# Kernel tuning notes

Hardware: AMD Instinct MI355X
Metric: run time of the kernel (lower is better)

## Reference

```python
import jax, jax.numpy as jnp
import numpy as np

L = 10      # LSTM layers
H = 128     # hidden size
ENC = 4096  # traffic_encoder_output_len
B = 8192    # batch
T = 12      # points_to_predict
NUM_MODES = 25


def setup_inputs() -> dict:
    key = jax.random.key(0)
    ks = jax.random.split(key, 10)
    s = 1.0 / np.sqrt(H)
    return {
        "backbone_encoded": jax.random.normal(ks[0], (B, ENC), jnp.float32),
        "fc_in_W": jax.random.normal(ks[1], (H, ENC), jnp.float32) / np.sqrt(ENC),
        "fc_in_b": jax.random.normal(ks[2], (H,), jnp.float32) * s,
        "Wih": jax.random.normal(ks[3], (L, 4 * H, H), jnp.float32) * s,
        "Whh": jax.random.normal(ks[4], (L, 4 * H, H), jnp.float32) * s,
        "bih": jax.random.normal(ks[5], (L, 4 * H), jnp.float32) * s,
        "bhh": jax.random.normal(ks[6], (L, 4 * H), jnp.float32) * s,
        "fc_out_W": jax.random.normal(ks[7], (3 * NUM_MODES, H), jnp.float32) * s,
        "fc_out_b": jax.random.normal(ks[8], (3 * NUM_MODES,), jnp.float32) * s,
        "points_to_predict": T,
    }


def _lstm_stack(x, Wih, Whh, bih, bhh):
    # x: [B, T, H]; PyTorch gate order: i, f, g, o
    def run_layer(x, l):
        def step(carry, xt):
            h, c = carry
            gates = xt @ Wih[l].T + h @ Whh[l].T + bih[l] + bhh[l]  # [B, 4H]
            i, f, g, o = jnp.split(gates, 4, axis=-1)
            c = jax.nn.sigmoid(f) * c + jax.nn.sigmoid(i) * jnp.tanh(g)
            h = jax.nn.sigmoid(o) * jnp.tanh(c)
            return (h, c), h
        b = x.shape[0]
        h0 = jnp.zeros((b, H), x.dtype)
        _, ys = jax.lax.scan(step, (h0, h0), jnp.swapaxes(x, 0, 1))  # [T, B, H]
        return jnp.swapaxes(ys, 0, 1)

    for l in range(L):
        x = run_layer(x, l)
    return x


def reference(backbone_encoded, fc_in_W, fc_in_b, Wih, Whh, bih, bhh,
              fc_out_W, fc_out_b, points_to_predict):
    enc = jax.nn.relu(backbone_encoded @ fc_in_W.T + fc_in_b)        # [B, H]
    x = jnp.repeat(enc[:, None, :], points_to_predict, axis=1)      # [B, T, H]
    y = _lstm_stack(x, Wih, Whh, bih, bhh)                           # [B, T, H]
    fc = y @ fc_out_W.T + fc_out_b                                   # [B, T, 75]
    b, t, _ = fc.shape
    # chunk(25, dim=channels) of consecutive pairs -> [B, 25, T, 2]
    predictions = fc[:, :, :50].reshape(b, t, NUM_MODES, 2).transpose(0, 2, 1, 3)
    probabilities = jax.nn.softmax(fc[:, -1, 50:], axis=-1)          # [B, 25]
    return predictions, probabilities
```

## Files before the change

kernel.cpp:

```cpp
#include <hip/hip_runtime.h>

typedef _Float16 h16;
typedef _Float16 h4 __attribute__((ext_vector_type(4)));
typedef _Float16 h8 __attribute__((ext_vector_type(8)));
typedef float f4 __attribute__((ext_vector_type(4)));

#define NB 8192
#define NENC 4096
#define NH 128
#define NL 10
#define NT 12
#define PAD 136

#define OFF_FCIN 0
#define SZ_FCIN (128*4096)
#define OFF_W (OFF_FCIN + SZ_FCIN)
#define SZ_W (10*2*512*128)
#define OFF_FCOUT (OFF_W + SZ_W)
#define SZ_FCOUT (80*128)
#define OFF_ENC (OFF_FCOUT + SZ_FCOUT)
#define SZ_ENC (8192*128)
#define OFF_GX0 (OFF_ENC + SZ_ENC)
#define SZ_GX0 (8192*512)
#define BYTE_BIAS ((OFF_GX0 + SZ_GX0)*2)

__device__ __forceinline__ f4 splat4(float v) { f4 r; r[0]=v; r[1]=v; r[2]=v; r[3]=v; return r; }
__device__ __forceinline__ h8 cvt8(float4 a, float4 b) {
  h8 r; r[0]=(h16)a.x; r[1]=(h16)a.y; r[2]=(h16)a.z; r[3]=(h16)a.w;
  r[4]=(h16)b.x; r[5]=(h16)b.y; r[6]=(h16)b.z; r[7]=(h16)b.w; return r;
}

__device__ __forceinline__ h16 cell(float iv, float fv, float gv, float ov, float& c) {
  float ei = __builtin_amdgcn_exp2f(-1.4426950408889634f * iv);
  float ef = __builtin_amdgcn_exp2f(-1.4426950408889634f * fv);
  float eg = __builtin_amdgcn_exp2f(-2.8853900817779268f * gv);
  float eo = __builtin_amdgcn_exp2f(-1.4426950408889634f * ov);
  float ai = 1.f + ei, af = 1.f + ef, ag = 1.f + eg;
  float m1 = ai * ag;
  float R1 = __builtin_amdgcn_rcpf(af * m1);
  float cc = R1 * fmaf(af, 1.f - eg, c * m1);
  c = cc;
  float ec = __builtin_amdgcn_exp2f(-2.8853900817779268f * cc);
  float R2 = __builtin_amdgcn_rcpf((1.f + eo) * (1.f + ec));
  return (h16)(R2 * (1.f - ec));
}

__global__ __launch_bounds__(256) void prep(const float* __restrict__ fcinW,
                                            const float* __restrict__ Wih,
                                            const float* __restrict__ Whh,
                                            const float* __restrict__ bih,
                                            const float* __restrict__ bhh,
                                            const float* __restrict__ fcoutW,
                                            h16* __restrict__ wsh,
                                            float* __restrict__ wbias) {
  int idx = blockIdx.x * 256 + threadIdx.x;
  if (idx < 65536) {
    int r = idx >> 9, k8 = idx & 511;
    const float* src = fcinW + r * 4096 + k8 * 8;
    h8 v = cvt8(*(const float4*)src, *(const float4*)(src + 4));
    *(h8*)(wsh + OFF_FCIN + (((r >> 4) * 512 + k8) * 128 + (r & 15) * 8)) = v;
  } else if (idx < 229376) {
    int rel = idx - 65536;
    int l = rel >> 14, rr = rel & 16383;
    int ssel = rr >> 13, rk8 = rr & 8191;
    int r = rk8 >> 4, k8 = rk8 & 15;
    const float* src = (ssel ? Whh : Wih) + l * 65536 + r * 128 + k8 * 8;
    h8 v = cvt8(*(const float4*)src, *(const float4*)(src + 4));
    *(h8*)(wsh + OFF_W + (l * 2 + ssel) * 65536 +
           (((r >> 4) * 16 + k8) * 128 + (r & 15) * 8)) = v;
  } else if (idx < 230656) {
    int rel = idx - 229376;
    int r = rel >> 4, k8 = rel & 15;
    h8 v;
    if (r < 75) {
      const float* src = fcoutW + r * 128 + k8 * 8;
      v = cvt8(*(const float4*)src, *(const float4*)(src + 4));
    } else {
      for (int j = 0; j < 8; ++j) v[j] = (h16)0.f;
    }
    *(h8*)(wsh + OFF_FCOUT + (((r >> 4) * 16 + k8) * 128 + (r & 15) * 8)) = v;
  } else if (idx < 235776) {
    int rel = idx - 230656;
    wbias[rel] = bih[rel] + bhh[rel];
  }
}

__global__ __launch_bounds__(256) void kin(const float* __restrict__ A,
                                           const float* __restrict__ bvec,
                                           h16* __restrict__ wsh) {
  const h16* Wp = wsh + OFF_FCIN;
  h16* ench = wsh + OFF_ENC;
  int tid = threadIdx.x;
  int w = tid >> 6, lane = tid & 63, s = lane & 15, q = lane >> 4;
  int m0 = blockIdx.x * 16;
  int c0 = w * 32 + s, c1 = c0 + 16;
  f4 acc0 = splat4(bvec[c0]);
  f4 acc1 = splat4(bvec[c1]);
  const float* arow = A + (size_t)(m0 + s) * NENC;
  const h16* wp0 = Wp + (w * 2 + 0) * (512 * 128) + s * 8;
  const h16* wp1 = Wp + (w * 2 + 1) * (512 * 128) + s * 8;
#pragma unroll 4
  for (int kb = 0; kb < 128; ++kb) {
    int k0 = kb * 32 + q * 8;
    float4 x0 = *(const float4*)(arow + k0);
    float4 x1 = *(const float4*)(arow + k0 + 4);
    h8 af = cvt8(x0, x1);
    h8 b0 = *(const h8*)(wp0 + (kb * 4 + q) * 128);
    h8 b1 = *(const h8*)(wp1 + (kb * 4 + q) * 128);
    acc0 = __builtin_amdgcn_mfma_f32_16x16x32_f16(af, b0, acc0, 0, 0, 0);
    acc1 = __builtin_amdgcn_mfma_f32_16x16x32_f16(af, b1, acc1, 0, 0, 0);
  }
#pragma unroll
  for (int r = 0; r < 4; ++r) {
    int b = m0 + q * 4 + r;
    float v0 = acc0[r]; v0 = v0 > 0.f ? v0 : 0.f;
    float v1 = acc1[r]; v1 = v1 > 0.f ? v1 : 0.f;
    ench[(size_t)b * NH + c0] = (h16)v0;
    ench[(size_t)b * NH + c1] = (h16)v1;
  }
}

__global__ __launch_bounds__(256) void kin2(h16* __restrict__ wsh,
                                            const float* __restrict__ wbias) {
  int tid = threadIdx.x;
  int w2 = tid >> 6, lane = tid & 63, s = lane & 15, q = lane >> 4;
  int bid = blockIdx.x;
  int lb = bid >> 3, mt = (bid >> 2) & 1, cg = bid & 3;
  const h16* ench = wsh + OFF_ENC;
  const h16* wih0 = wsh + OFF_W;
  h16* gx0 = wsh + OFF_GX0;
  const h16* arow = ench + (size_t)(lb * 32 + mt * 16 + s) * NH;
  h8 ax[4];
#pragma unroll
  for (int kt = 0; kt < 4; ++kt) ax[kt] = *(const h8*)(arow + kt * 32 + q * 8);
#pragma unroll
  for (int ti = 0; ti < 2; ++ti) {
    int W = w2 * 2 + ti;
    int rb = cg * 8 + W;
    f4 acc = splat4(wbias[cg * 128 + W * 16 + s]);
#pragma unroll
    for (int kt = 0; kt < 4; ++kt) {
      h8 b = *(const h8*)(wih0 + (rb * 16 + kt * 4 + q) * 128 + s * 8);
      acc = __builtin_amdgcn_mfma_f32_16x16x32_f16(ax[kt], b, acc, 0, 0, 0);
    }
    h4 st; st[0] = (h16)acc[0]; st[1] = (h16)acc[1]; st[2] = (h16)acc[2]; st[3] = (h16)acc[3];
    *(h4*)(gx0 + ((((size_t)lb * 8 + W) * 8 + cg * 2 + mt) * 64 + lane) * 4) = st;
  }
}

__global__ __launch_bounds__(512, 2) void lstm(h16* __restrict__ wsh,
                                               const float* __restrict__ wbias,
                                               const float* __restrict__ fcoutb,
                                               float* __restrict__ out) {
  __shared__ h16 ring[13][32][PAD];
  __shared__ float probst[32 * 26];
  int tid = threadIdx.x;
  int w = tid >> 6, lane = tid & 63, s = lane & 15, q = lane >> 4;
  int brow = blockIdx.x * 32;
  h8 wx[4][4], wh[4][4];
  float bb[4];
  float c[2][4];

  {
    const h16* whh = wsh + OFF_W + 65536;
#pragma unroll
    for (int g = 0; g < 4; ++g)
#pragma unroll
      for (int kt = 0; kt < 4; ++kt)
        wh[g][kt] = *(const h8*)(whh + (((g * 8 + w) * 16 + kt * 4 + q) * 128) + s * 8);
    f4 gx[4][2];
    const h16* gxp = wsh + OFF_GX0 + ((size_t)blockIdx.x * 8 + w) * 8 * 256 + (size_t)lane * 4;
#pragma unroll
    for (int g = 0; g < 4; ++g)
#pragma unroll
      for (int mt = 0; mt < 2; ++mt) {
        h4 v = *(const h4*)(gxp + (g * 2 + mt) * 256);
        f4 a; a[0] = (float)v[0]; a[1] = (float)v[1]; a[2] = (float)v[2]; a[3] = (float)v[3];
        gx[g][mt] = a;
      }
#pragma unroll
    for (int mt = 0; mt < 2; ++mt)
#pragma unroll
      for (int r = 0; r < 4; ++r) c[mt][r] = 0.f;
    for (int t = 0; t < NT; ++t) {
      __syncthreads();
      int rw = t + 11; if (rw >= 13) rw -= 13;
      int rh = t + 10; if (rh >= 13) rh -= 13;
      f4 acc[4][2];
#pragma unroll
      for (int g = 0; g < 4; ++g)
#pragma unroll
        for (int mt = 0; mt < 2; ++mt) acc[g][mt] = gx[g][mt];
      if (t > 0) {
#pragma unroll
        for (int mt = 0; mt < 2; ++mt) {
          h8 ah[4];
#pragma unroll
          for (int kt = 0; kt < 4; ++kt)
            ah[kt] = *(const h8*)&ring[rh][mt * 16 + s][kt * 32 + q * 8];
#pragma unroll
          for (int g = 0; g < 4; ++g)
#pragma unroll
            for (int kt = 0; kt < 4; ++kt)
              acc[g][mt] = __builtin_amdgcn_mfma_f32_16x16x32_f16(ah[kt], wh[g][kt], acc[g][mt], 0, 0, 0);
        }
      }
#pragma unroll
      for (int mt = 0; mt < 2; ++mt)
#pragma unroll
        for (int r = 0; r < 4; ++r) {
          h16 hv = cell(acc[0][mt][r], acc[1][mt][r], acc[2][mt][r], acc[3][mt][r], c[mt][r]);
          ring[rw][mt * 16 + q * 4 + r][w * 16 + s] = hv;
        }
    }
  }
  for (int l = 1; l < NL; ++l) {
    const h16* wih = wsh + OFF_W + (size_t)(l * 2) * 65536;
    const h16* whh = wih + 65536;
#pragma unroll
    for (int g = 0; g < 4; ++g) {
#pragma unroll
      for (int kt = 0; kt < 4; ++kt) {
        int off = (((g * 8 + w) * 16 + kt * 4 + q) * 128) + s * 8;
        wx[g][kt] = *(const h8*)(wih + off);
        wh[g][kt] = *(const h8*)(whh + off);
      }
      bb[g] = wbias[l * 512 + g * 128 + w * 16 + s];
    }
    f4 acc[4][2];
#pragma unroll
    for (int g = 0; g < 4; ++g)
#pragma unroll
      for (int mt = 0; mt < 2; ++mt) acc[g][mt] = splat4(bb[g]);
#pragma unroll
    for (int mt = 0; mt < 2; ++mt)
#pragma unroll
      for (int r = 0; r < 4; ++r) c[mt][r] = 0.f;
    for (int t = 0; t < NT; ++t) {
      __syncthreads();
      int rw = t + 11 - l; if (rw >= 13) rw -= 13;
      if (t == 0) {
        int rr = rw + 1; if (rr >= 13) rr -= 13;
#pragma unroll
        for (int mt = 0; mt < 2; ++mt) {
          h8 ax[4];
#pragma unroll
          for (int kt = 0; kt < 4; ++kt)
            ax[kt] = *(const h8*)&ring[rr][mt * 16 + s][kt * 32 + q * 8];
#pragma unroll
          for (int g = 0; g < 4; ++g)
#pragma unroll
            for (int kt = 0; kt < 4; ++kt)
              acc[g][mt] = __builtin_amdgcn_mfma_f32_16x16x32_f16(ax[kt], wx[g][kt], acc[g][mt], 0, 0, 0);
        }
      } else {
        int rh = rw - 1; if (rh < 0) rh += 13;
#pragma unroll
        for (int mt = 0; mt < 2; ++mt) {
          h8 ah[4];
#pragma unroll
          for (int kt = 0; kt < 4; ++kt)
            ah[kt] = *(const h8*)&ring[rh][mt * 16 + s][kt * 32 + q * 8];
#pragma unroll
          for (int g = 0; g < 4; ++g)
#pragma unroll
            for (int kt = 0; kt < 4; ++kt)
              acc[g][mt] = __builtin_amdgcn_mfma_f32_16x16x32_f16(ah[kt], wh[g][kt], acc[g][mt], 0, 0, 0);
        }
      }
      int rx = rw + 2; if (rx >= 13) rx -= 13;
#pragma unroll
      for (int mt = 0; mt < 2; ++mt) {
        h8 axn[4];
#pragma unroll
        for (int kt = 0; kt < 4; ++kt)
          axn[kt] = *(const h8*)&ring[rx][mt * 16 + s][kt * 32 + q * 8];
        h16 hv[4];
#pragma unroll
        for (int r = 0; r < 4; ++r)
          hv[r] = cell(acc[0][mt][r], acc[1][mt][r], acc[2][mt][r], acc[3][mt][r], c[mt][r]);
#pragma unroll
        for (int g = 0; g < 4; ++g) acc[g][mt] = splat4(bb[g]);
#pragma unroll
        for (int g = 0; g < 4; ++g)
#pragma unroll
          for (int kt = 0; kt < 4; ++kt)
            acc[g][mt] = __builtin_amdgcn_mfma_f32_16x16x32_f16(axn[kt], wx[g][kt], acc[g][mt], 0, 0, 0);
#pragma unroll
        for (int r = 0; r < 4; ++r)
          ring[rw][mt * 16 + q * 4 + r][w * 16 + s] = hv[r];
      }
    }
  }
  __syncthreads();
  h8 wo[5][4];
  float bo[5];
  const h16* fco = wsh + OFF_FCOUT;
#pragma unroll
  for (int nt = 0; nt < 5; ++nt) {
#pragma unroll
    for (int kt = 0; kt < 4; ++kt)
      wo[nt][kt] = *(const h8*)(fco + (nt * 16 + kt * 4 + q) * 128 + s * 8);
    int col = nt * 16 + s;
    bo[nt] = (col < 75) ? fcoutb[col] : 0.f;
  }
  int tcount = (w < 4) ? 2 : 1;
  for (int ti = 0; ti < tcount; ++ti) {
    int t = w + ti * 8;
    int sl = t + 2; if (sl >= 13) sl -= 13;
#pragma unroll
    for (int mt = 0; mt < 2; ++mt) {
      h8 ax[4];
#pragma unroll
      for (int kt = 0; kt < 4; ++kt)
        ax[kt] = *(const h8*)&ring[sl][mt * 16 + s][kt * 32 + q * 8];
#pragma unroll
      for (int nt = 0; nt < 5; ++nt) {
        f4 a = splat4(bo[nt]);
#pragma unroll
        for (int kt = 0; kt < 4; ++kt)
          a = __builtin_amdgcn_mfma_f32_16x16x32_f16(ax[kt], wo[nt][kt], a, 0, 0, 0);
        int col = nt * 16 + s;
#pragma unroll
        for (int r = 0; r < 4; ++r) {
          int row = mt * 16 + q * 4 + r;
          int b = brow + row;
          float v = a[r];
          if (col < 50)
            out[(size_t)b * 600 + (col >> 1) * 24 + t * 2 + (col & 1)] = v;
          if (t == 11 && col >= 50 && col < 75)
            probst[row * 26 + (col - 50)] = v;
        }
      }
    }
  }
  __syncthreads();
  if (tid < 32) {
    float vals[25];
    float m = -1e30f;
#pragma unroll
    for (int j = 0; j < 25; ++j) { vals[j] = probst[tid * 26 + j]; m = vals[j] > m ? vals[j] : m; }
    float sum = 0.f;
#pragma unroll
    for (int j = 0; j < 25; ++j) {
      float e = __builtin_amdgcn_exp2f((vals[j] - m) * 1.4426950408889634f);
      vals[j] = e; sum += e;
    }
    float rs = 1.0f / sum;
    size_t pb = (size_t)4915200 + (size_t)(brow + tid) * 25;
#pragma unroll
    for (int j = 0; j < 25; ++j) out[pb + j] = vals[j] * rs;
  }
}

extern "C" void kernel_launch(void* const* d_in, const int* in_sizes, int n_in,
                              void* d_out, int out_size, void* d_ws, size_t ws_size,
                              hipStream_t stream) {
  const float* backbone = (const float*)d_in[0];
  const float* fcinW    = (const float*)d_in[1];
  const float* fcinb    = (const float*)d_in[2];
  const float* Wih      = (const float*)d_in[3];
  const float* Whh      = (const float*)d_in[4];
  const float* bih      = (const float*)d_in[5];
  const float* bhh      = (const float*)d_in[6];
  const float* fcoutW   = (const float*)d_in[7];
  const float* fcoutb   = (const float*)d_in[8];
  h16* wsh = (h16*)d_ws;
  float* wbias = (float*)((char*)d_ws + BYTE_BIAS);

  prep<<<922, 256, 0, stream>>>(fcinW, Wih, Whh, bih, bhh, fcoutW, wsh, wbias);
  kin<<<512, 256, 0, stream>>>(backbone, fcinb, wsh);
  kin2<<<2048, 256, 0, stream>>>(wsh, wbias);
  lstm<<<256, 512, 0, stream>>>(wsh, wbias, fcoutb, (float*)d_out);
}
```

Before: 498.7 us.

## Fold sigmoid/tanh exponent scaling into LSTM weights and restructure ring addressing

Prescales the LSTM input/hidden weights and combined biases by -log2(e), or -2·log2(e) for the g gate, during prep. The cell can then call exp2 directly on the gate pre-activations without per-element multiplies. The shared-memory ring is reordered to [row][slot][col] with precomputed per-lane read/write base pointers, which cuts index arithmetic. Layer 0's first timestep is peeled, and bias/gx are passed directly as the first MFMA accumulator. Rounding weights to fp16 after scaling changes numerics slightly.

```diff
diff --git a/kernel.cpp b/kernel.cpp
--- a/kernel.cpp
+++ b/kernel.cpp
@@ -11,6 +11,8 @@
 #define NL 10
 #define NT 12
 #define PAD 136
+#define L2E 1.4426950408889634f
+#define K2 -2.8853900817779268f
 
 #define OFF_FCIN 0
 #define SZ_FCIN (128*4096)
@@ -29,18 +31,22 @@
   h8 r; r[0]=(h16)a.x; r[1]=(h16)a.y; r[2]=(h16)a.z; r[3]=(h16)a.w;
   r[4]=(h16)b.x; r[5]=(h16)b.y; r[6]=(h16)b.z; r[7]=(h16)b.w; return r;
 }
+__device__ __forceinline__ h8 cvt8s(float4 a, float4 b, float sc) {
+  h8 r; r[0]=(h16)(a.x*sc); r[1]=(h16)(a.y*sc); r[2]=(h16)(a.z*sc); r[3]=(h16)(a.w*sc);
+  r[4]=(h16)(b.x*sc); r[5]=(h16)(b.y*sc); r[6]=(h16)(b.z*sc); r[7]=(h16)(b.w*sc); return r;
+}
 
 __device__ __forceinline__ h16 cell(float iv, float fv, float gv, float ov, float& c) {
-  float ei = __builtin_amdgcn_exp2f(-1.4426950408889634f * iv);
-  float ef = __builtin_amdgcn_exp2f(-1.4426950408889634f * fv);
-  float eg = __builtin_amdgcn_exp2f(-2.8853900817779268f * gv);
-  float eo = __builtin_amdgcn_exp2f(-1.4426950408889634f * ov);
+  float ei = __builtin_amdgcn_exp2f(iv);
+  float ef = __builtin_amdgcn_exp2f(fv);
+  float eg = __builtin_amdgcn_exp2f(gv);
+  float eo = __builtin_amdgcn_exp2f(ov);
   float ai = 1.f + ei, af = 1.f + ef, ag = 1.f + eg;
   float m1 = ai * ag;
   float R1 = __builtin_amdgcn_rcpf(af * m1);
   float cc = R1 * fmaf(af, 1.f - eg, c * m1);
   c = cc;
-  float ec = __builtin_amdgcn_exp2f(-2.8853900817779268f * cc);
+  float ec = __builtin_amdgcn_exp2f(K2 * cc);
   float R2 = __builtin_amdgcn_rcpf((1.f + eo) * (1.f + ec));
   return (h16)(R2 * (1.f - ec));
 }
@@ -64,8 +70,9 @@
     int l = rel >> 14, rr = rel & 16383;
     int ssel = rr >> 13, rk8 = rr & 8191;
     int r = rk8 >> 4, k8 = rk8 & 15;
+    float sc = ((r >> 7) == 2) ? (-2.f * L2E) : (-L2E);
     const float* src = (ssel ? Whh : Wih) + l * 65536 + r * 128 + k8 * 8;
-    h8 v = cvt8(*(const float4*)src, *(const float4*)(src + 4));
+    h8 v = cvt8s(*(const float4*)src, *(const float4*)(src + 4), sc);
     *(h8*)(wsh + OFF_W + (l * 2 + ssel) * 65536 +
            (((r >> 4) * 16 + k8) * 128 + (r & 15) * 8)) = v;
   } else if (idx < 230656) {
@@ -81,7 +88,9 @@
     *(h8*)(wsh + OFF_FCOUT + (((r >> 4) * 16 + k8) * 128 + (r & 15) * 8)) = v;
   } else if (idx < 235776) {
     int rel = idx - 230656;
-    wbias[rel] = bih[rel] + bhh[rel];
+    int col = rel & 511;
+    float sc = ((col >> 7) == 2) ? (-2.f * L2E) : (-L2E);
+    wbias[rel] = (bih[rel] + bhh[rel]) * sc;
   }
 }
 
@@ -152,14 +161,19 @@
                                                const float* __restrict__ wbias,
                                                const float* __restrict__ fcoutb,
                                                float* __restrict__ out) {
-  __shared__ h16 ring[13][32][PAD];
+  __shared__ h16 ring[32][13][PAD];
   __shared__ float probst[32 * 26];
   int tid = threadIdx.x;
   int w = tid >> 6, lane = tid & 63, s = lane & 15, q = lane >> 4;
   int brow = blockIdx.x * 32;
   h8 wx[4][4], wh[4][4];
-  float bb[4];
+  f4 bbv[4];
   float c[2][4];
+  h16* rd0 = &ring[s][0][q * 8];
+  h16* rd1 = &ring[16 + s][0][q * 8];
+  h16* wr0 = &ring[q * 4][0][w * 16 + s];
+  h16* wr1 = &ring[16 + q * 4][0][w * 16 + s];
+#define RSTRIDE (13 * PAD)
 
   {
     const h16* whh = wsh + OFF_W + 65536;
@@ -182,36 +196,48 @@
     for (int mt = 0; mt < 2; ++mt)
 #pragma unroll
       for (int r = 0; r < 4; ++r) c[mt][r] = 0.f;
-    for (int t = 0; t < NT; ++t) {
+    {
+      h16* q0 = wr0 + 11 * PAD;
+      h16* q1 = wr1 + 11 * PAD;
+#pragma unroll
+      for (int mt = 0; mt < 2; ++mt) {
+        h16* qq = mt ? q1 : q0;
+#pragma unroll
+        for (int r = 0; r < 4; ++r)
+          qq[r * RSTRIDE] = cell(gx[0][mt][r], gx[1][mt][r], gx[2][mt][r], gx[3][mt][r], c[mt][r]);
+      }
+    }
+    int rw = 12;
+    for (int t = 1; t < NT; ++t) {
       __syncthreads();
-      int rw = t + 11; if (rw >= 13) rw -= 13;
-      int rh = t + 10; if (rh >= 13) rh -= 13;
+      int rh = rw - 1; if (rh < 0) rh += 13;
       f4 acc[4][2];
-#pragma unroll
-      for (int g = 0; g < 4; ++g)
-#pragma unroll
-        for (int mt = 0; mt < 2; ++mt) acc[g][mt] = gx[g][mt];
-      if (t > 0) {
-#pragma unroll
-        for (int mt = 0; mt < 2; ++mt) {
-          h8 ah[4];
-#pragma unroll
-          for (int kt = 0; kt < 4; ++kt)
-            ah[kt] = *(const h8*)&ring[rh][mt * 16 + s][kt * 32 + q * 8];
-#pragma unroll
-          for (int g = 0; g < 4; ++g)
-#pragma unroll
-            for (int kt = 0; kt < 4; ++kt)
-              acc[g][mt] = __builtin_amdgcn_mfma_f32_16x16x32_f16(ah[kt], wh[g][kt], acc[g][mt], 0, 0, 0);
+      const h16* p0 = rd0 + rh * PAD;
+      const h16* p1 = rd1 + rh * PAD;
+#pragma unroll
+      for (int mt = 0; mt < 2; ++mt) {
+        const h16* pp = mt ? p1 : p0;
+        h8 ah[4];
+#pragma unroll
+        for (int kt = 0; kt < 4; ++kt) ah[kt] = *(const h8*)(pp + kt * 32);
+#pragma unroll
+        for (int g = 0; g < 4; ++g) {
+          acc[g][mt] = __builtin_amdgcn_mfma_f32_16x16x32_f16(ah[0], wh[g][0], gx[g][mt], 0, 0, 0);
+#pragma unroll
+          for (int kt = 1; kt < 4; ++kt)
+            acc[g][mt] = __builtin_amdgcn_mfma_f32_16x16x32_f16(ah[kt], wh[g][kt], acc[g][mt], 0, 0, 0);
         }
       }
-#pragma unroll
-      for (int mt = 0; mt < 2; ++mt)
-#pragma unroll
-        for (int r = 0; r < 4; ++r) {
-          h16 hv = cell(acc[0][mt][r], acc[1][mt][r], acc[2][mt][r], acc[3][mt][r], c[mt][r]);
-          ring[rw][mt * 16 + q * 4 + r][w * 16 + s] = hv;
-        }
+      h16* q0 = wr0 + rw * PAD;
+      h16* q1 = wr1 + rw * PAD;
+#pragma unroll
+      for (int mt = 0; mt < 2; ++mt) {
+        h16* qq = mt ? q1 : q0;
+#pragma unroll
+        for (int r = 0; r < 4; ++r)
+          qq[r * RSTRIDE] = cell(acc[0][mt][r], acc[1][mt][r], acc[2][mt][r], acc[3][mt][r], c[mt][r]);
+      }
+      ++rw; if (rw >= 13) rw = 0;
     }
   }
   for (int l = 1; l < NL; ++l) {
@@ -225,42 +251,44 @@
         wx[g][kt] = *(const h8*)(wih + off);
         wh[g][kt] = *(const h8*)(whh + off);
       }
-      bb[g] = wbias[l * 512 + g * 128 + w * 16 + s];
-    }
+      bbv[g] = splat4(wbias[l * 512 + g * 128 + w * 16 + s]);
+    }
+#pragma unroll
+    for (int mt = 0; mt < 2; ++mt)
+#pragma unroll
+      for (int r = 0; r < 4; ++r) c[mt][r] = 0.f;
+    int rw = 11 - l;
     f4 acc[4][2];
-#pragma unroll
-    for (int g = 0; g < 4; ++g)
-#pragma unroll
-      for (int mt = 0; mt < 2; ++mt) acc[g][mt] = splat4(bb[g]);
-#pragma unroll
-    for (int mt = 0; mt < 2; ++mt)
-#pragma unroll
-      for (int r = 0; r < 4; ++r) c[mt][r] = 0.f;
+    {
+      const h16* p0 = rd0 + (rw + 1) * PAD;
+      const h16* p1 = rd1 + (rw + 1) * PAD;
+#pragma unroll
+      for (int mt = 0; mt < 2; ++mt) {
+        const h16* pp = mt ? p1 : p0;
+        h8 ax[4];
+#pragma unroll
+        for (int kt = 0; kt < 4; ++kt) ax[kt] = *(const h8*)(pp + kt * 32);
+#pragma unroll
+        for (int g = 0; g < 4; ++g) {
+          acc[g][mt] = __builtin_amdgcn_mfma_f32_16x16x32_f16(ax[0], wx[g][0], bbv[g], 0, 0, 0);
+#pragma unroll
+          for (int kt = 1; kt < 4; ++kt)
+            acc[g][mt] = __builtin_amdgcn_mfma_f32_16x16x32_f16(ax[kt], wx[g][kt], acc[g][mt], 0, 0, 0);
+        }
+      }
+    }
     for (int t = 0; t < NT; ++t) {
       __syncthreads();
-      int rw = t + 11 - l; if (rw >= 13) rw -= 13;
-      if (t == 0) {
-        int rr = rw + 1; if (rr >= 13) rr -= 13;
+      if (t > 0) {
+        int rh = rw - 1; if (rh < 0) rh += 13;
+        const h16* p0 = rd0 + rh * PAD;
+        const h16* p1 = rd1 + rh * PAD;
 #pragma unroll
         for (int mt = 0; mt < 2; ++mt) {
-          h8 ax[4];
-#pragma unroll
-          for (int kt = 0; kt < 4; ++kt)
-            ax[kt] = *(const h8*)&ring[rr][mt * 16 + s][kt * 32 + q * 8];
-#pragma unroll
-          for (int g = 0; g < 4; ++g)
-#pragma unroll
-            for (int kt = 0; kt < 4; ++kt)
-              acc[g][mt] = __builtin_amdgcn_mfma_f32_16x16x32_f16(ax[kt], wx[g][kt], acc[g][mt], 0, 0, 0);
-        }
-      } else {
-        int rh = rw - 1; if (rh < 0) rh += 13;
-#pragma unroll
-        for (int mt = 0; mt < 2; ++mt) {
+          const h16* pp = mt ? p1 : p0;
           h8 ah[4];
 #pragma unroll
-          for (int kt = 0; kt < 4; ++kt)
-            ah[kt] = *(const h8*)&ring[rh][mt * 16 + s][kt * 32 + q * 8];
+          for (int kt = 0; kt < 4; ++kt) ah[kt] = *(const h8*)(pp + kt * 32);
 #pragma unroll
           for (int g = 0; g < 4; ++g)
 #pragma unroll
@@ -268,28 +296,40 @@
               acc[g][mt] = __builtin_amdgcn_mfma_f32_16x16x32_f16(ah[kt], wh[g][kt], acc[g][mt], 0, 0, 0);
         }
       }
-      int rx = rw + 2; if (rx >= 13) rx -= 13;
-#pragma unroll
-      for (int mt = 0; mt < 2; ++mt) {
-        h8 axn[4];
-#pragma unroll
-        for (int kt = 0; kt < 4; ++kt)
-          axn[kt] = *(const h8*)&ring[rx][mt * 16 + s][kt * 32 + q * 8];
-        h16 hv[4];
+      h16 hv[2][4];
+#pragma unroll
+      for (int mt = 0; mt < 2; ++mt)
 #pragma unroll
         for (int r = 0; r < 4; ++r)
-          hv[r] = cell(acc[0][mt][r], acc[1][mt][r], acc[2][mt][r], acc[3][mt][r], c[mt][r]);
-#pragma unroll
-        for (int g = 0; g < 4; ++g) acc[g][mt] = splat4(bb[g]);
-#pragma unroll
-        for (int g = 0; g < 4; ++g)
-#pragma unroll
-          for (int kt = 0; kt < 4; ++kt)
-            acc[g][mt] = __builtin_amdgcn_mfma_f32_16x16x32_f16(axn[kt], wx[g][kt], acc[g][mt], 0, 0, 0);
-#pragma unroll
-        for (int r = 0; r < 4; ++r)
-          ring[rw][mt * 16 + q * 4 + r][w * 16 + s] = hv[r];
-      }
+          hv[mt][r] = cell(acc[0][mt][r], acc[1][mt][r], acc[2][mt][r], acc[3][mt][r], c[mt][r]);
+      if (t < 11) {
+        int rx = rw + 2; if (rx >= 13) rx -= 13;
+        const h16* p0 = rd0 + rx * PAD;
+        const h16* p1 = rd1 + rx * PAD;
+#pragma unroll
+        for (int mt = 0; mt < 2; ++mt) {
+          const h16* pp = mt ? p1 : p0;
+          h8 ax[4];
+#pragma unroll
+          for (int kt = 0; kt < 4; ++kt) ax[kt] = *(const h8*)(pp + kt * 32);
+#pragma unroll
+          for (int g = 0; g < 4; ++g) {
+            acc[g][mt] = __builtin_amdgcn_mfma_f32_16x16x32_f16(ax[0], wx[g][0], bbv[g], 0, 0, 0);
+#pragma unroll
+            for (int kt = 1; kt < 4; ++kt)
+              acc[g][mt] = __builtin_amdgcn_mfma_f32_16x16x32_f16(ax[kt], wx[g][kt], acc[g][mt], 0, 0, 0);
+          }
+        }
+      }
+      h16* q0 = wr0 + rw * PAD;
+      h16* q1 = wr1 + rw * PAD;
+#pragma unroll
+      for (int mt = 0; mt < 2; ++mt) {
+        h16* qq = mt ? q1 : q0;
+#pragma unroll
+        for (int r = 0; r < 4; ++r) qq[r * RSTRIDE] = hv[mt][r];
+      }
+      ++rw; if (rw >= 13) rw = 0;
     }
   }
   __syncthreads();
@@ -310,10 +350,10 @@
     int sl = t + 2; if (sl >= 13) sl -= 13;
 #pragma unroll
     for (int mt = 0; mt < 2; ++mt) {
+      const h16* pp = (mt ? rd1 : rd0) + sl * PAD;
       h8 ax[4];
 #pragma unroll
-      for (int kt = 0; kt < 4; ++kt)
-        ax[kt] = *(const h8*)&ring[sl][mt * 16 + s][kt * 32 + q * 8];
+      for (int kt = 0; kt < 4; ++kt) ax[kt] = *(const h8*)(pp + kt * 32);
 #pragma unroll
       for (int nt = 0; nt < 5; ++nt) {
         f4 a = splat4(bo[nt]);
@@ -343,7 +383,7 @@
     float sum = 0.f;
 #pragma unroll
     for (int j = 0; j < 25; ++j) {
-      float e = __builtin_amdgcn_exp2f((vals[j] - m) * 1.4426950408889634f);
+      float e = __builtin_amdgcn_exp2f((vals[j] - m) * L2E);
       vals[j] = e; sum += e;
     }
     float rs = 1.0f / sum;
```

Result: no change. 494.1 us (-0.9%).
